# Optimization experiments

Hardware: AMD Instinct MI355X
Metric: run time of the kernel (lower is better)

## Reference

```python
import jax, jax.numpy as jnp
import numpy as np

N_LEVELS = 8
N_FEATS = 2
LOG2_T = 19
BASE_RES = 16.0
FINEST_RES = 2048.0
BOX_MIN, BOX_MAX = 0.0, 1.0
B_GROWTH = float(np.exp((np.log(FINEST_RES) - np.log(BASE_RES)) / (N_LEVELS - 1)))  # = 2.0
HASH_MASK = (1 << LOG2_T) - 1
BATCH = 4194304


def setup_inputs() -> dict:
    key = jax.random.key(0)
    kx, kt = jax.random.split(key)
    x = jax.random.uniform(kx, (BATCH, 1), dtype=jnp.float32, minval=BOX_MIN, maxval=BOX_MAX)
    # n_levels separate embedding tables, init uniform in [-1e-4, 1e-4]
    tables = jax.random.uniform(kt, (N_LEVELS, 1 << LOG2_T, N_FEATS), dtype=jnp.float32,
                                minval=-1e-4, maxval=1e-4)
    return {"x": x, "tables": tables}


def reference(x, tables):
    # x: [B, 1] in [BOX_MIN, BOX_MAX]; tables: [L, 2^T, F]
    outs = []
    for i in range(N_LEVELS):
        resolution = jnp.floor(BASE_RES * (B_GROWTH ** i))
        grid_size = (BOX_MAX - BOX_MIN) / resolution
        idx = jnp.floor((x - BOX_MIN) / grid_size)            # [B, 1] cell index (float)
        interval_min = BOX_MIN + idx * grid_size              # [B, 1]
        interval_max = interval_min + grid_size               # [B, 1]
        # two interval vertices: idx and idx+1; 1-D spatial hash = index & (2^T - 1)
        verts = jnp.concatenate([idx, idx + 1.0], axis=-1).astype(jnp.int32)  # [B, 2]
        hashed = jnp.bitwise_and(verts, HASH_MASK)            # [B, 2]
        emb = tables[i][hashed]                               # [B, 2, F] gather
        w = (x - interval_min) / (interval_max - interval_min)  # [B, 1]
        c = emb[:, 0] * (1.0 - w) + emb[:, 1] * w             # [B, F]
        outs.append(c)
    return jnp.concatenate(outs, axis=-1)                     # [B, L*F]
```

## Files before the change

kernel.cpp:

```cpp
#include <hip/hip_runtime.h>


#define NGP_BATCH   4194304
#define NGP_TSIZE   (1 << 19)
#define BLOCK       512
#define PPB         2048
#define KITER       (PPB / (BLOCK/4))
#define NBODY       (KITER / 4)

typedef float f32x4 __attribute__((ext_vector_type(4)));

__global__ __launch_bounds__(BLOCK) void hashenc_kernel(
    const float* __restrict__ x,
    const float* __restrict__ tables,
    float* __restrict__ out)
{
    __shared__ float2 sm[4088];

    const int tid = threadIdx.x;

#pragma unroll
    for (int l = 0; l < 8; ++l) {
        const int n   = (16 << l) + 1;
        const int off = 16 * ((1 << l) - 1) + l;
        const float2* __restrict__ src =
            reinterpret_cast<const float2*>(tables) + (size_t)l * NGP_TSIZE;
        for (int e = tid; e < n; e += BLOCK)
            sm[off + e] = src[e];
    }
    __syncthreads();

    const int q  = tid >> 2;
    const int s  = tid & 3;
    const int l0 = 2 * s;
    const int l1 = 2 * s + 1;
    const float res0 = (float)(16 << l0);
    const float res1 = (float)(16 << l1);
    const int   off0 = 16 * ((1 << l0) - 1) + l0;
    const int   off1 = 16 * ((1 << l1) - 1) + l1;

    const int P0 = blockIdx.x * PPB;
    f32x4* __restrict__ out4 = reinterpret_cast<f32x4*>(out);

    float xc[4], xn[4];
#pragma unroll
    for (int j = 0; j < 4; ++j)
        xc[j] = x[P0 + q + 128 * j];

#pragma unroll
    for (int m = 0; m < NBODY; ++m) {
        if (m + 1 < NBODY) {
#pragma unroll
            for (int j = 0; j < 4; ++j)
                xn[j] = x[P0 + q + 128 * (4 * (m + 1) + j)];
        }

#pragma unroll
        for (int j = 0; j < 4; ++j) {
            const int   p  = P0 + q + 128 * (4 * m + j);
            const float xv = xc[j];

            const float fx0 = xv * res0;
            const float fi0 = floorf(fx0);
            const float w0  = fx0 - fi0;
            const int   i0  = off0 + (int)fi0;
            const float2 a0 = sm[i0];
            const float2 b0 = sm[i0 + 1];

            const float fx1 = xv * res1;
            const float fi1 = floorf(fx1);
            const float w1  = fx1 - fi1;
            const int   i1  = off1 + (int)fi1;
            const float2 a1 = sm[i1];
            const float2 b1 = sm[i1 + 1];

            f32x4 r;
            r.x = fmaf(w0, b0.x - a0.x, a0.x);
            r.y = fmaf(w0, b0.y - a0.y, a0.y);
            r.z = fmaf(w1, b1.x - a1.x, a1.x);
            r.w = fmaf(w1, b1.y - a1.y, a1.y);

            __builtin_nontemporal_store(r, &out4[(size_t)p * 4 + s]);
        }

        if (m + 1 < NBODY) {
#pragma unroll
            for (int j = 0; j < 4; ++j)
                xc[j] = xn[j];
        }
    }
}

extern "C" void kernel_launch(void* const* d_in, const int* in_sizes, int n_in,
                              void* d_out, int out_size, void* d_ws, size_t ws_size,
                              hipStream_t stream) {
    const float* x      = (const float*)d_in[0];
    const float* tables = (const float*)d_in[1];
    float*       out    = (float*)d_out;

    const int grid = NGP_BATCH / PPB;
    hashenc_kernel<<<grid, BLOCK, 0, stream>>>(x, tables, out);
}
```

Before: 54.20 us.

## Store per-cell value and delta as float4 in LDS, double points per block

The shared-memory table now holds one float4 per cell: the left vertex features plus the precomputed difference to the right vertex. Each lookup becomes a single 128-bit LDS read with no subtraction, replacing two float2 reads. Points per block double, so the table staging cost is spread over more points, but there are half as many blocks. The LDS footprint also roughly doubles, to about 65 KB, which may lower occupancy.

```diff
diff --git a/kernel.cpp b/kernel.cpp
--- a/kernel.cpp
+++ b/kernel.cpp
@@ -4,7 +4,7 @@
 #define NGP_BATCH   4194304
 #define NGP_TSIZE   (1 << 19)
 #define BLOCK       512
-#define PPB         2048
+#define PPB         4096
 #define KITER       (PPB / (BLOCK/4))
 #define NBODY       (KITER / 4)
 
@@ -15,18 +15,21 @@
     const float* __restrict__ tables,
     float* __restrict__ out)
 {
-    __shared__ float2 sm[4088];
+    __shared__ float4 sm4[4080];
 
     const int tid = threadIdx.x;
 
 #pragma unroll
     for (int l = 0; l < 8; ++l) {
-        const int n   = (16 << l) + 1;
-        const int off = 16 * ((1 << l) - 1) + l;
+        const int n   = 16 << l;
+        const int off = 16 * ((1 << l) - 1);
         const float2* __restrict__ src =
             reinterpret_cast<const float2*>(tables) + (size_t)l * NGP_TSIZE;
-        for (int e = tid; e < n; e += BLOCK)
-            sm[off + e] = src[e];
+        for (int e = tid; e < n; e += BLOCK) {
+            const float2 a = src[e];
+            const float2 b = src[e + 1];
+            sm4[off + e] = make_float4(a.x, a.y, b.x - a.x, b.y - a.y);
+        }
     }
     __syncthreads();
 
@@ -36,8 +39,8 @@
     const int l1 = 2 * s + 1;
     const float res0 = (float)(16 << l0);
     const float res1 = (float)(16 << l1);
-    const int   off0 = 16 * ((1 << l0) - 1) + l0;
-    const int   off1 = 16 * ((1 << l1) - 1) + l1;
+    const int   off0 = 16 * ((1 << l0) - 1);
+    const int   off1 = 16 * ((1 << l1) - 1);
 
     const int P0 = blockIdx.x * PPB;
     f32x4* __restrict__ out4 = reinterpret_cast<f32x4*>(out);
@@ -63,22 +66,18 @@
             const float fx0 = xv * res0;
             const float fi0 = floorf(fx0);
             const float w0  = fx0 - fi0;
-            const int   i0  = off0 + (int)fi0;
-            const float2 a0 = sm[i0];
-            const float2 b0 = sm[i0 + 1];
+            const float4 e0 = sm4[off0 + (int)fi0];
 
             const float fx1 = xv * res1;
             const float fi1 = floorf(fx1);
             const float w1  = fx1 - fi1;
-            const int   i1  = off1 + (int)fi1;
-            const float2 a1 = sm[i1];
-            const float2 b1 = sm[i1 + 1];
+            const float4 e1 = sm4[off1 + (int)fi1];
 
             f32x4 r;
-            r.x = fmaf(w0, b0.x - a0.x, a0.x);
-            r.y = fmaf(w0, b0.y - a0.y, a0.y);
-            r.z = fmaf(w1, b1.x - a1.x, a1.x);
-            r.w = fmaf(w1, b1.y - a1.y, a1.y);
+            r.x = fmaf(w0, e0.z, e0.x);
+            r.y = fmaf(w0, e0.w, e0.y);
+            r.z = fmaf(w1, e1.z, e1.x);
+            r.w = fmaf(w1, e1.w, e1.y);
 
             __builtin_nontemporal_store(r, &out4[(size_t)p * 4 + s]);
         }
```

New measurement: 51.55 us, median of 2. 4.9% less time.
